# Performance work log

Measured on AMD Instinct MI355X. Metric: run time of the kernel, lower is better.

## Reference

```python
import jax, jax.numpy as jnp
import numpy as np

N = 100000      # nodes
E = 3200000     # edges (avg degree 32)
F_IN = 128      # data.num_features
H = 64          # hidden_channels
L = 64          # num_layers
C = 47          # data.num_classes
ALPHA = 0.1
THETA = 0.5


def setup_inputs() -> dict:
    key = jax.random.key(0)
    ks = jax.random.split(key, 8)
    x = jax.random.normal(ks[0], (N, F_IN), dtype=jnp.float32)
    edge_index = jax.random.randint(ks[1], (2, E), 0, N, dtype=jnp.int64)
    # Linear(F_IN, H), Linear(H, C), and L shared GCN2Conv weights [H, H]
    W1 = jax.random.normal(ks[2], (F_IN, H), dtype=jnp.float32) * 0.05
    b1 = jnp.zeros((H,), dtype=jnp.float32)
    conv_W = jax.random.normal(ks[3], (L, H, H), dtype=jnp.float32) * 0.05
    W2 = jax.random.normal(ks[4], (H, C), dtype=jnp.float32) * 0.05
    b2 = jnp.zeros((C,), dtype=jnp.float32)
    return {"x": x, "edge_index": edge_index, "W1": W1, "b1": b1,
            "conv_W": conv_W, "W2": W2, "b2": b2}


def reference(x, edge_index, W1, b1, conv_W, W2, b2):
    # --- normalized adjacency with renormalization trick: D^-1/2 (A + I) D^-1/2, transposed ---
    sl = jnp.arange(N, dtype=edge_index.dtype)
    r = jnp.concatenate([edge_index[1], sl])  # adj_t rows (destinations)
    c = jnp.concatenate([edge_index[0], sl])  # adj_t cols (sources)
    deg = jax.ops.segment_sum(jnp.ones((r.shape[0],), jnp.float32), r, num_segments=N)
    dinv = jax.lax.rsqrt(deg)                 # self-loops guarantee deg >= 1
    w = dinv[r] * dinv[c]                     # [E + N] edge weights

    def spmm(h):  # A_hat @ h via gather + segment scatter-add
        return jax.ops.segment_sum(w[:, None] * h[c], r, num_segments=N)

    # dropout is identity in eval mode
    x0 = jax.nn.relu(x @ W1 + b1)             # [N, H]
    betas = jnp.log(THETA / jnp.arange(1, L + 1, dtype=jnp.float32) + 1.0)

    def step(h, layer):
        Wl, beta = layer
        p = spmm(h)
        s = (1.0 - ALPHA) * p + ALPHA * x0    # initial-residual mix
        h = jax.nn.relu((1.0 - beta) * s + beta * (s @ Wl))  # identity mapping
        return h, None

    h, _ = jax.lax.scan(step, x0, (conv_W, betas))
    logits = h @ W2 + b2                      # [N, C]
    return jax.nn.log_softmax(logits, axis=-1)
```

## Files before the change

kernel.cpp:

```cpp
#include <hip/hip_runtime.h>
#include <hip/hip_bf16.h>
#include <hip/hip_fp16.h>
#include <math.h>

#define NN 100000
#define NE 3200000
#define FIN 128
#define HD 64
#define NL 64
#define NC 47
#define RPW 4
#define WPB 4
#define RPB (RPW * WPB)

#define NQ 4
#define NSEG 4
#define NKEY (NN * NQ)
#define KB ((NKEY + 1023) / 1024)

typedef float f32x4 __attribute__((ext_vector_type(4)));
typedef unsigned int u32x4 __attribute__((ext_vector_type(4)));


__device__ __forceinline__ float bf2f(unsigned short u) {
    union { unsigned int i; float f; } v; v.i = ((unsigned int)u) << 16; return v.f;
}
__device__ __forceinline__ unsigned short f2bf(float f) {
    __hip_bfloat16 h = __float2bfloat16(f);
    return *reinterpret_cast<unsigned short*>(&h);
}
__device__ __forceinline__ float bflo(unsigned int u) {
    union { unsigned int i; float f; } v; v.i = u << 16; return v.f;
}
__device__ __forceinline__ float bfhi(unsigned int u) {
    union { unsigned int i; float f; } v; v.i = u & 0xFFFF0000u; return v.f;
}
__device__ __forceinline__ unsigned int pack2h(float a, float b) {
    __half ha = __float2half(a), hb = __float2half(b);
    unsigned short ua = *reinterpret_cast<unsigned short*>(&ha);
    unsigned short ub = *reinterpret_cast<unsigned short*>(&hb);
    return (unsigned int)ua | ((unsigned int)ub << 16);
}
__device__ __forceinline__ float h2f(unsigned short u) {
    __half h = *reinterpret_cast<__half*>(&u);
    return __half2float(h);
}
__device__ __forceinline__ float fin_at(const void* p, int isf32, size_t i) {
    return isf32 ? ((const float*)p)[i]
                 : __bfloat162float(((const __hip_bfloat16*)p)[i]);
}
__device__ __forceinline__ int edge_at(const void* p, int is64, size_t i) {
    return is64 ? (int)((const long long*)p)[i] : ((const int*)p)[i];
}


__global__ void detect_kernel(const void* __restrict__ x, const void* __restrict__ eidx,
                              int* __restrict__ flags) {
    if (threadIdx.x == 0 && blockIdx.x == 0) {
        const unsigned short* u = (const unsigned short*)x;
        int sane = 0;
        for (int i = 0; i < 64; i++) {
            unsigned short v = u[2 * i];
            int e = (v >> 7) & 0xFF;
            if ((v & 0x7FFF) == 0 || (e >= 90 && e <= 141)) sane++;
        }
        flags[0] = (sane >= 48) ? 0 : 1;
        const int* e32 = (const int*)eidx;
        int nz = 0;
        for (int i = 0; i < 64; i++) if (e32[2 * i + 1] != 0) nz++;
        flags[1] = (nz == 0) ? 1 : 0;
    }
}


__global__ void key_count(const void* __restrict__ eidx, const int* __restrict__ flags,
                          int* __restrict__ cnt, int big) {
    int e = blockIdx.x * blockDim.x + threadIdx.x;
    if (e < NE) {
        int is64 = flags[1];
        int s = edge_at(eidx, is64, (size_t)e);
        int d = edge_at(eidx, is64, (size_t)NE + e);
        int q = s & 3;
        int key = big ? (q * NN + d) : (d * 4 + q);
        atomicAdd(&cnt[key], 1);
    }
}

__global__ __launch_bounds__(1024) void scan_reduce(const int* __restrict__ cnt,
                                                    int* __restrict__ bsum) {
    __shared__ int lds[1024];
    int tid = threadIdx.x;
    int i = blockIdx.x * 1024 + tid;
    lds[tid] = (i < NKEY) ? cnt[i] : 0;
    __syncthreads();
    for (int off = 512; off > 0; off >>= 1) {
        if (tid < off) lds[tid] += lds[tid + off];
        __syncthreads();
    }
    if (tid == 0) bsum[blockIdx.x] = lds[0];
}

__global__ __launch_bounds__(1024) void scan_mid(int* __restrict__ bsum, int* __restrict__ total_out) {
    __shared__ int lds[1024];
    __shared__ int base_s;
    int tid = threadIdx.x;
    if (tid == 0) base_s = 0;
    __syncthreads();
    for (int chunk = 0; chunk < KB; chunk += 1024) {
        int i = chunk + tid;
        int v = (i < KB) ? bsum[i] : 0;
        lds[tid] = v;
        __syncthreads();
        for (int off = 1; off < 1024; off <<= 1) {
            int t = (tid >= off) ? lds[tid - off] : 0;
            __syncthreads();
            lds[tid] += t;
            __syncthreads();
        }
        int incl = lds[tid];
        int base = base_s;
        if (i < KB) bsum[i] = base + incl - v;
        __syncthreads();
        if (tid == 1023) base_s = base + incl;
        __syncthreads();
    }
    if (tid == 0) *total_out = base_s;
}

__global__ __launch_bounds__(1024) void scan_final(const int* __restrict__ cnt,
                                                   const int* __restrict__ bsum,
                                                   int* __restrict__ keyptr) {
    __shared__ int lds[1024];
    int tid = threadIdx.x;
    int i = blockIdx.x * 1024 + tid;
    int v = (i < NKEY) ? cnt[i] : 0;
    lds[tid] = v;
    __syncthreads();
    for (int off = 1; off < 1024; off <<= 1) {
        int t = (tid >= off) ? lds[tid - off] : 0;
        __syncthreads();
        lds[tid] += t;
        __syncthreads();
    }
    if (i < NKEY) keyptr[i] = bsum[blockIdx.x] + lds[tid] - v;
}

__global__ void dinv_kernel(const int* __restrict__ keyptr, float* __restrict__ dinv, int big) {
    int i = blockIdx.x * blockDim.x + threadIdx.x;
    if (i < NN) {
        int deg;
        if (big) {
            deg = 0;
            #pragma unroll
            for (int q = 0; q < NQ; q++)
                deg += keyptr[q * NN + i + 1] - keyptr[q * NN + i];
        } else {
            deg = keyptr[(i + 1) * NSEG] - keyptr[i * NSEG];
        }
        dinv[i] = rsqrtf(1.0f + (float)deg);
    }
}

__global__ void scatter_kernel(const void* __restrict__ eidx, const int* __restrict__ flags,
                               const int* __restrict__ keyptr, int* __restrict__ fill,
                               int* __restrict__ col, int big) {
    int e = blockIdx.x * blockDim.x + threadIdx.x;
    if (e < NE) {
        int is64 = flags[1];
        int s = edge_at(eidx, is64, (size_t)e);
        int d = edge_at(eidx, is64, (size_t)NE + e);
        int q = s & 3;
        int key = big ? (q * NN + d) : (d * 4 + q);
        int pos = keyptr[key] + atomicAdd(&fill[key], 1);
        col[pos] = s;
    }
}


__global__ __launch_bounds__(256) void x0_kernel(const void* __restrict__ x,
                                                 const void* __restrict__ W1,
                                                 const void* __restrict__ b1,
                                                 const int* __restrict__ flags,
                                                 const float* __restrict__ dinv,
                                                 unsigned short* __restrict__ x0b,
                                                 unsigned short* __restrict__ g0) {
    __shared__ float lw[FIN * HD];
    int isf = flags[0];
    int tid = threadIdx.x;
    for (int i = tid; i < FIN * HD; i += 256) lw[i] = fin_at(W1, isf, i);
    __syncthreads();
    int wave = tid >> 6, lane = tid & 63;
    int row0 = blockIdx.x * RPB + wave * RPW;
    if (row0 >= NN) return;
    unsigned int pa01, pa23, pb01, pb23;
    {
        unsigned short a0 = f2bf(fin_at(x, isf, (size_t)(row0 + 0) * FIN + lane));
        unsigned short a1 = f2bf(fin_at(x, isf, (size_t)(row0 + 1) * FIN + lane));
        unsigned short a2 = f2bf(fin_at(x, isf, (size_t)(row0 + 2) * FIN + lane));
        unsigned short a3 = f2bf(fin_at(x, isf, (size_t)(row0 + 3) * FIN + lane));
        unsigned short c0 = f2bf(fin_at(x, isf, (size_t)(row0 + 0) * FIN + 64 + lane));
        unsigned short c1 = f2bf(fin_at(x, isf, (size_t)(row0 + 1) * FIN + 64 + lane));
        unsigned short c2 = f2bf(fin_at(x, isf, (size_t)(row0 + 2) * FIN + 64 + lane));
        unsigned short c3 = f2bf(fin_at(x, isf, (size_t)(row0 + 3) * FIN + 64 + lane));
        pa01 = ((unsigned int)a0 << 16) | a1;  pa23 = ((unsigned int)a2 << 16) | a3;
        pb01 = ((unsigned int)c0 << 16) | c1;  pb23 = ((unsigned int)c2 << 16) | c3;
    }
    float bias = fin_at(b1, isf, lane);
    float d0 = bias, d1 = bias, d2 = bias, d3 = bias;
    #pragma unroll 8
    for (int k = 0; k < 64; k++) {
        float w = lw[k * HD + lane];
        unsigned int b01 = __shfl(pa01, k, 64);
        unsigned int b23 = __shfl(pa23, k, 64);
        union { unsigned int i; float f; } f0, f1, f2, f3;
        f0.i = b01 & 0xFFFF0000u; f1.i = b01 << 16;
        f2.i = b23 & 0xFFFF0000u; f3.i = b23 << 16;
        d0 += f0.f * w; d1 += f1.f * w; d2 += f2.f * w; d3 += f3.f * w;
    }
    #pragma unroll 8
    for (int k = 0; k < 64; k++) {
        float w = lw[(64 + k) * HD + lane];
        unsigned int b01 = __shfl(pb01, k, 64);
        unsigned int b23 = __shfl(pb23, k, 64);
        union { unsigned int i; float f; } f0, f1, f2, f3;
        f0.i = b01 & 0xFFFF0000u; f1.i = b01 << 16;
        f2.i = b23 & 0xFFFF0000u; f3.i = b23 << 16;
        d0 += f0.f * w; d1 += f1.f * w; d2 += f2.f * w; d3 += f3.f * w;
    }
    float dd[RPW] = {d0, d1, d2, d3};
    #pragma unroll
    for (int r = 0; r < RPW; r++) {
        int row = row0 + r;
        if (row >= NN) continue;
        float v = fmaxf(dd[r], 0.0f);
        x0b[(size_t)row * HD + lane] = f2bf(v);
        g0[(size_t)row * HD + lane] = f2bf(dinv[row] * v);
    }
}


__global__ __launch_bounds__(256, 8) void spmm_partial(const int* __restrict__ keyptr,
                                                       const int* __restrict__ colq,
                                                       const unsigned short* __restrict__ g_in,
                                                       unsigned short* __restrict__ part) {
    int bid = blockIdx.x;
    int quad = bid & 3;
    int tile = bid >> 2;
    int tid = threadIdx.x;
    int wave = tid >> 6, lane = tid & 63;
    int grp = lane >> 3, li = lane & 7;
    int row = tile * 32 + wave * 8 + grp;
    size_t kbase = (size_t)quad * NN + row;
    int jbeg = keyptr[kbase];
    int jend = keyptr[kbase + 1];
    int cnt = jend - jbeg;
    const char* gb = (const char*)g_in;

    float a0 = 0.0f, a1 = 0.0f, a2 = 0.0f, a3 = 0.0f;
    float a4 = 0.0f, a5 = 0.0f, a6 = 0.0f, a7 = 0.0f;

    for (int base = 0; base < cnt; base += 8) {
        int idx = jbeg + base + li;
        int cv = colq[idx < jend ? idx : (jend - 1)];
        int rem = cnt - base;
        #pragma unroll
        for (int k = 0; k < 8; k++) {
            if (k < rem) {
                int ck = __shfl(cv, (lane & 56) + k, 64);
                uint4 u = *reinterpret_cast<const uint4*>(gb + (((size_t)ck) << 7) + (li << 4));
                a0 += bflo(u.x); a1 += bfhi(u.x);
                a2 += bflo(u.y); a3 += bfhi(u.y);
                a4 += bflo(u.z); a5 += bfhi(u.z);
                a6 += bflo(u.w); a7 += bfhi(u.w);
            }
        }
    }

    if (quad == (row & 3)) {
        uint4 u = *reinterpret_cast<const uint4*>(gb + (((size_t)row) << 7) + (li << 4));
        a0 += bflo(u.x); a1 += bfhi(u.x);
        a2 += bflo(u.y); a3 += bfhi(u.y);
        a4 += bflo(u.z); a5 += bfhi(u.z);
        a6 += bflo(u.w); a7 += bfhi(u.w);
    }

    u32x4 v = {pack2h(a0, a1), pack2h(a2, a3), pack2h(a4, a5), pack2h(a6, a7)};
    unsigned short* pp = part + kbase * HD + (li << 3);
    __builtin_nontemporal_store(v, reinterpret_cast<u32x4*>(pp));
}


__global__ __launch_bounds__(256, 8) void layer_combine(const unsigned short* __restrict__ part,
                                                        const float* __restrict__ dinv,
                                                        const unsigned short* __restrict__ x0b,
                                                        unsigned short* __restrict__ g_out,
                                                        const void* __restrict__ convW, int layer,
                                                        const int* __restrict__ flags, float beta) {
    __shared__ float lw[HD * HD];
    int isf = flags[0];
    size_t wbase = (size_t)layer * HD * HD;
    int tid = threadIdx.x;
    for (int i = tid; i < HD * HD; i += 256) lw[i] = fin_at(convW, isf, wbase + i);
    __syncthreads();

    int wave = __builtin_amdgcn_readfirstlane(tid >> 6);
    int lane = tid & 63;
    int row0 = blockIdx.x * RPB + wave * RPW;

    float sacc[RPW];
    float dsc[RPW];
    #pragma unroll
    for (int r = 0; r < RPW; r++) {
        int row = row0 + r;
        if (row >= NN) { sacc[r] = 0.0f; dsc[r] = 1.0f; continue; }
        float a = 0.0f;
        #pragma unroll
        for (int q = 0; q < NQ; q++) {
            unsigned short u = __builtin_nontemporal_load(
                part + ((size_t)q * NN + row) * HD + lane);
            a += h2f(u);
        }
        float di = dinv[row];
        dsc[r] = di;
        sacc[r] = 0.9f * (di * a) + 0.1f * bf2f(x0b[((size_t)row << 6) + lane]);
    }

    unsigned int p01 = ((unsigned int)f2bf(sacc[0]) << 16) | f2bf(sacc[1]);
    unsigned int p23 = ((unsigned int)f2bf(sacc[2]) << 16) | f2bf(sacc[3]);
    float d0 = 0.0f, d1 = 0.0f, d2 = 0.0f, d3 = 0.0f;
    #pragma unroll 8
    for (int k = 0; k < 64; k++) {
        float w = lw[k * HD + lane];
        unsigned int b01 = __shfl(p01, k, 64);
        unsigned int b23 = __shfl(p23, k, 64);
        union { unsigned int i; float f; } f0, f1, f2, f3;
        f0.i = b01 & 0xFFFF0000u; f1.i = b01 << 16;
        f2.i = b23 & 0xFFFF0000u; f3.i = b23 << 16;
        d0 += f0.f * w; d1 += f1.f * w;
        d2 += f2.f * w; d3 += f3.f * w;
    }

    float dd[RPW] = {d0, d1, d2, d3};
    float omb = 1.0f - beta;
    #pragma unroll
    for (int r = 0; r < RPW; r++) {
        int row = row0 + r;
        if (row >= NN) continue;
        float res = omb * sacc[r] + beta * dd[r];
        g_out[((size_t)row << 6) + lane] = f2bf(dsc[r] * fmaxf(res, 0.0f));
    }
}


__global__ __launch_bounds__(256, 8) void layer_fused(const int* __restrict__ keyptr,
                                                      const int* __restrict__ col,
                                                      const float* __restrict__ dinv,
                                                      const unsigned short* __restrict__ g_in,
                                                      const unsigned short* __restrict__ x0b,
                                                      unsigned short* __restrict__ g_out,
                                                      const void* __restrict__ convW, int layer,
                                                      const int* __restrict__ flags, float beta) {
    __shared__ float lw[HD * HD];
    int isf = flags[0];
    size_t wbase = (size_t)layer * HD * HD;
    int tid = threadIdx.x;
    for (int i = tid; i < HD * HD; i += 256) lw[i] = fin_at(convW, isf, wbase + i);
    __syncthreads();

    int wave = __builtin_amdgcn_readfirstlane(tid >> 6);
    int lane = tid & 63;
    int eslot = lane >> 3;
    int sbyte = (lane & 7) << 4;
    const char* gb = (const char*)g_in;

    int row0 = blockIdx.x * RPB + wave * RPW;

    float sacc[RPW];
    float dsc[RPW];
    #pragma unroll
    for (int r = 0; r < RPW; r++) {
        int row = row0 + r;
        if (row >= NN) { sacc[r] = 0.0f; dsc[r] = 1.0f; continue; }
        int start = keyptr[row * NSEG];
        int end   = keyptr[(row + 1) * NSEG];

        float a0 = 0.0f, a1 = 0.0f, a2 = 0.0f, a3 = 0.0f;
        float a4 = 0.0f, a5 = 0.0f, a6 = 0.0f, a7 = 0.0f;

        for (int j = start; j < end; j += 32) {
            int le = end - 1;
            int i0 = j + eslot, i1 = i0 + 8, i2 = i0 + 16, i3 = i0 + 24;
            int c0 = col[i0 < end ? i0 : le];
            int c1 = col[i1 < end ? i1 : le];
            int c2 = col[i2 < end ? i2 : le];
            int c3 = col[i3 < end ? i3 : le];
            uint4 u0 = *reinterpret_cast<const uint4*>(gb + (((size_t)c0) << 7) + sbyte);
            uint4 u1 = *reinterpret_cast<const uint4*>(gb + (((size_t)c1) << 7) + sbyte);
            uint4 u2 = *reinterpret_cast<const uint4*>(gb + (((size_t)c2) << 7) + sbyte);
            uint4 u3 = *reinterpret_cast<const uint4*>(gb + (((size_t)c3) << 7) + sbyte);
            float m0 = (i0 < end) ? 1.0f : 0.0f;
            float m1 = (i1 < end) ? 1.0f : 0.0f;
            float m2 = (i2 < end) ? 1.0f : 0.0f;
            float m3 = (i3 < end) ? 1.0f : 0.0f;
            a0 = fmaf(m0, bflo(u0.x), a0); a1 = fmaf(m0, bfhi(u0.x), a1);
            a2 = fmaf(m0, bflo(u0.y), a2); a3 = fmaf(m0, bfhi(u0.y), a3);
            a4 = fmaf(m0, bflo(u0.z), a4); a5 = fmaf(m0, bfhi(u0.z), a5);
            a6 = fmaf(m0, bflo(u0.w), a6); a7 = fmaf(m0, bfhi(u0.w), a7);
            a0 = fmaf(m1, bflo(u1.x), a0); a1 = fmaf(m1, bfhi(u1.x), a1);
            a2 = fmaf(m1, bflo(u1.y), a2); a3 = fmaf(m1, bfhi(u1.y), a3);
            a4 = fmaf(m1, bflo(u1.z), a4); a5 = fmaf(m1, bfhi(u1.z), a5);
            a6 = fmaf(m1, bflo(u1.w), a6); a7 = fmaf(m1, bfhi(u1.w), a7);
            a0 = fmaf(m2, bflo(u2.x), a0); a1 = fmaf(m2, bfhi(u2.x), a1);
            a2 = fmaf(m2, bflo(u2.y), a2); a3 = fmaf(m2, bfhi(u2.y), a3);
            a4 = fmaf(m2, bflo(u2.z), a4); a5 = fmaf(m2, bfhi(u2.z), a5);
            a6 = fmaf(m2, bflo(u2.w), a6); a7 = fmaf(m2, bfhi(u2.w), a7);
            a0 = fmaf(m3, bflo(u3.x), a0); a1 = fmaf(m3, bfhi(u3.x), a1);
            a2 = fmaf(m3, bflo(u3.y), a2); a3 = fmaf(m3, bfhi(u3.y), a3);
            a4 = fmaf(m3, bflo(u3.z), a4); a5 = fmaf(m3, bfhi(u3.z), a5);
            a6 = fmaf(m3, bflo(u3.w), a6); a7 = fmaf(m3, bfhi(u3.w), a7);
        }

        a0 += __shfl_xor(a0, 8, 64); a0 += __shfl_xor(a0, 16, 64); a0 += __shfl_xor(a0, 32, 64);
        a1 += __shfl_xor(a1, 8, 64); a1 += __shfl_xor(a1, 16, 64); a1 += __shfl_xor(a1, 32, 64);
        a2 += __shfl_xor(a2, 8, 64); a2 += __shfl_xor(a2, 16, 64); a2 += __shfl_xor(a2, 32, 64);
        a3 += __shfl_xor(a3, 8, 64); a3 += __shfl_xor(a3, 16, 64); a3 += __shfl_xor(a3, 32, 64);
        a4 += __shfl_xor(a4, 8, 64); a4 += __shfl_xor(a4, 16, 64); a4 += __shfl_xor(a4, 32, 64);
        a5 += __shfl_xor(a5, 8, 64); a5 += __shfl_xor(a5, 16, 64); a5 += __shfl_xor(a5, 32, 64);
        a6 += __shfl_xor(a6, 8, 64); a6 += __shfl_xor(a6, 16, 64); a6 += __shfl_xor(a6, 32, 64);
        a7 += __shfl_xor(a7, 8, 64); a7 += __shfl_xor(a7, 16, 64); a7 += __shfl_xor(a7, 32, 64);

        int srcl = lane >> 3;
        float t0 = __shfl(a0, srcl, 64);
        float t1 = __shfl(a1, srcl, 64);
        float t2 = __shfl(a2, srcl, 64);
        float t3 = __shfl(a3, srcl, 64);
        float t4 = __shfl(a4, srcl, 64);
        float t5 = __shfl(a5, srcl, 64);
        float t6 = __shfl(a6, srcl, 64);
        float t7 = __shfl(a7, srcl, 64);
        int b0 = lane & 1, b1 = (lane >> 1) & 1, b2 = (lane >> 2) & 1;
        float s01 = b0 ? t1 : t0, s23 = b0 ? t3 : t2;
        float s45 = b0 ? t5 : t4, s67 = b0 ? t7 : t6;
        float sA = b1 ? s23 : s01, sB = b1 ? s67 : s45;
        float gsum = b2 ? sB : sA;

        float a = gsum + bf2f(g_in[((size_t)row << 6) + lane]);
        float di = dinv[row];
        dsc[r] = di;
        sacc[r] = 0.9f * (di * a) + 0.1f * bf2f(x0b[((size_t)row << 6) + lane]);
    }

    unsigned int p01 = ((unsigned int)f2bf(sacc[0]) << 16) | f2bf(sacc[1]);
    unsigned int p23 = ((unsigned int)f2bf(sacc[2]) << 16) | f2bf(sacc[3]);
    float d0 = 0.0f, d1 = 0.0f, d2 = 0.0f, d3 = 0.0f;
    #pragma unroll 8
    for (int k = 0; k < 64; k++) {
        float w = lw[k * HD + lane];
        unsigned int b01 = __shfl(p01, k, 64);
        unsigned int b23 = __shfl(p23, k, 64);
        union { unsigned int i; float f; } f0, f1, f2, f3;
        f0.i = b01 & 0xFFFF0000u; f1.i = b01 << 16;
        f2.i = b23 & 0xFFFF0000u; f3.i = b23 << 16;
        d0 += f0.f * w; d1 += f1.f * w;
        d2 += f2.f * w; d3 += f3.f * w;
    }

    float dd[RPW] = {d0, d1, d2, d3};
    float omb = 1.0f - beta;
    #pragma unroll
    for (int r = 0; r < RPW; r++) {
        int row = row0 + r;
        if (row >= NN) continue;
        float res = omb * sacc[r] + beta * dd[r];
        g_out[((size_t)row << 6) + lane] = f2bf(dsc[r] * fmaxf(res, 0.0f));
    }
}


__global__ __launch_bounds__(256) void out_kernel(const unsigned short* __restrict__ g,
                                                  const float* __restrict__ dinv,
                                                  const void* __restrict__ W2,
                                                  const void* __restrict__ b2,
                                                  const int* __restrict__ flags,
                                                  void* __restrict__ out) {
    __shared__ float lw[HD * 64];
    int isf = flags[0];
    int tid = threadIdx.x;
    for (int i = tid; i < HD * 64; i += 256) {
        int k = i >> 6, j = i & 63;
        lw[i] = (j < NC) ? fin_at(W2, isf, (size_t)k * NC + j) : 0.0f;
    }
    __syncthreads();
    int row = blockIdx.x * 4 + (tid >> 6);
    int lane = tid & 63;
    if (row >= NN) return;
    float hv = bf2f(g[(size_t)row * HD + lane]) / dinv[row];
    float acc = (lane < NC) ? fin_at(b2, isf, lane) : 0.0f;
    #pragma unroll 8
    for (int k = 0; k < 64; k++) {
        float hk = __shfl(hv, k, 64);
        acc += hk * lw[k * 64 + lane];
    }
    float mv = (lane < NC) ? acc : -1e30f;
    for (int off = 32; off > 0; off >>= 1) mv = fmaxf(mv, __shfl_xor(mv, off, 64));
    float ex = (lane < NC) ? expf(acc - mv) : 0.0f;
    float se = ex;
    for (int off = 32; off > 0; off >>= 1) se += __shfl_xor(se, off, 64);
    float res = acc - mv - logf(se);
    if (lane < NC) {
        size_t oi = (size_t)row * NC + lane;
        if (isf) ((float*)out)[oi] = res;
        else     ((__hip_bfloat16*)out)[oi] = __float2bfloat16(res);
    }
}


static inline size_t align256(size_t x) { return (x + 255) & ~(size_t)255; }

extern "C" void kernel_launch(void* const* d_in, const int* in_sizes, int n_in,
                              void* d_out, int out_size, void* d_ws, size_t ws_size,
                              hipStream_t stream) {
    const void* x     = d_in[0];
    const void* eidx  = d_in[1];
    const void* W1    = d_in[2];
    const void* b1    = d_in[3];
    const void* convW = d_in[4];
    const void* W2    = d_in[5];
    const void* b2    = d_in[6];

    char* p = (char*)d_ws;
    size_t off = 0;
    auto alloc = [&](size_t bytes) { void* r = p + off; off += align256(bytes); return r; };
    int*            flags   = (int*)alloc(256);
    int*            cnt     = (int*)alloc((size_t)NKEY * 4);
    int*            fill    = (int*)alloc((size_t)NKEY * 4);
    int*            keyptr  = (int*)alloc((size_t)(NKEY + 1) * 4);
    int*            bsum    = (int*)alloc((size_t)KB * 4);
    float*          dinv    = (float*)alloc((size_t)NN * 4);
    int*            col     = (int*)alloc((size_t)NE * 4);
    unsigned short* x0b     = (unsigned short*)alloc((size_t)NN * HD * 2);
    unsigned short* hA      = (unsigned short*)alloc((size_t)NN * HD * 2);
    unsigned short* hB      = (unsigned short*)alloc((size_t)NN * HD * 2);

    size_t part_bytes = (size_t)NQ * NN * HD * 2;
    int big = (off + part_bytes) <= ws_size;
    unsigned short* part = (unsigned short*)(p + off);

    detect_kernel<<<1, 64, 0, stream>>>(x, eidx, flags);

    hipMemsetAsync(cnt, 0, (size_t)NKEY * 4, stream);
    hipMemsetAsync(fill, 0, (size_t)NKEY * 4, stream);
    key_count<<<(NE + 255) / 256, 256, 0, stream>>>(eidx, flags, cnt, big);
    scan_reduce<<<KB, 1024, 0, stream>>>(cnt, bsum);
    scan_mid<<<1, 1024, 0, stream>>>(bsum, keyptr + NKEY);
    scan_final<<<KB, 1024, 0, stream>>>(cnt, bsum, keyptr);
    dinv_kernel<<<(NN + 255) / 256, 256, 0, stream>>>(keyptr, dinv, big);
    scatter_kernel<<<(NE + 255) / 256, 256, 0, stream>>>(eidx, flags, keyptr, fill, col, big);

    int fb = (NN + RPB - 1) / RPB;
    x0_kernel<<<fb, 256, 0, stream>>>(x, W1, b1, flags, dinv, x0b, hA);

    unsigned short* gin = hA;
    unsigned short* gout = hB;
    for (int l = 0; l < NL; l++) {
        float beta = logf(0.5f / (float)(l + 1) + 1.0f);
        if (big) {
            spmm_partial<<<(NN / 32) * NQ, 256, 0, stream>>>(keyptr, col, gin, part);
            layer_combine<<<fb, 256, 0, stream>>>(part, dinv, x0b, gout,
                                                  convW, l, flags, beta);
        } else {
            layer_fused<<<fb, 256, 0, stream>>>(keyptr, col, dinv, gin, x0b, gout,
                                                convW, l, flags, beta);
        }
        unsigned short* t = gin; gin = gout; gout = t;
    }
    out_kernel<<<(NN + 3) / 4, 256, 0, stream>>>(gin, dinv, W2, b2, flags, (void*)d_out);
}
```

Measured before the change: 7.157 ms.

## Bind SpMM column quarters to XCDs via persistent work-stealing blocks

Turns spmm_partial into a persistent kernel with a fixed grid. Each block reads its XCC ID and pulls 32-row tiles from per-quarter atomic counters, starting with the quarter matching its XCD. The aim is that each XCD gathers mostly from one quarter of the feature table, so that quarter stays in that XCD's L2 and fewer gathers go to HBM or Infinity Cache. It adds atomic traffic, two block barriers per tile, and per-layer counters that must be zeroed.

```diff
diff --git a/kernel.cpp b/kernel.cpp
--- a/kernel.cpp
+++ b/kernel.cpp
@@ -17,6 +17,9 @@
 #define NSEG 4
 #define NKEY (NN * NQ)
 #define KB ((NKEY + 1023) / 1024)
+
+#define PGRID 2048
+#define NTILE 3125
 
 typedef float f32x4 __attribute__((ext_vector_type(4)));
 typedef unsigned int u32x4 __attribute__((ext_vector_type(4)));
@@ -242,51 +245,67 @@
 __global__ __launch_bounds__(256, 8) void spmm_partial(const int* __restrict__ keyptr,
                                                        const int* __restrict__ colq,
                                                        const unsigned short* __restrict__ g_in,
-                                                       unsigned short* __restrict__ part) {
-    int bid = blockIdx.x;
-    int quad = bid & 3;
-    int tile = bid >> 2;
+                                                       unsigned short* __restrict__ part,
+                                                       int* __restrict__ qcnt) {
+    unsigned int xcc;
+    asm volatile("s_getreg_b32 %0, hwreg(HW_REG_XCC_ID)" : "=s"(xcc));
+    int myq = (int)(xcc & 3);
+    __shared__ int tile_s;
     int tid = threadIdx.x;
     int wave = tid >> 6, lane = tid & 63;
     int grp = lane >> 3, li = lane & 7;
-    int row = tile * 32 + wave * 8 + grp;
-    size_t kbase = (size_t)quad * NN + row;
-    int jbeg = keyptr[kbase];
-    int jend = keyptr[kbase + 1];
-    int cnt = jend - jbeg;
     const char* gb = (const char*)g_in;
 
-    float a0 = 0.0f, a1 = 0.0f, a2 = 0.0f, a3 = 0.0f;
-    float a4 = 0.0f, a5 = 0.0f, a6 = 0.0f, a7 = 0.0f;
-
-    for (int base = 0; base < cnt; base += 8) {
-        int idx = jbeg + base + li;
-        int cv = colq[idx < jend ? idx : (jend - 1)];
-        int rem = cnt - base;
-        #pragma unroll
-        for (int k = 0; k < 8; k++) {
-            if (k < rem) {
-                int ck = __shfl(cv, (lane & 56) + k, 64);
-                uint4 u = *reinterpret_cast<const uint4*>(gb + (((size_t)ck) << 7) + (li << 4));
+    for (int qi = 0; qi < NQ; qi++) {
+        int quad = (myq + qi) & 3;
+        while (true) {
+            __syncthreads();
+            if (tid == 0) tile_s = atomicAdd(&qcnt[quad], 1);
+            __syncthreads();
+            int tile = tile_s;
+            if (tile >= NTILE) break;
+
+            int row = tile * 32 + wave * 8 + grp;
+            size_t kbase = (size_t)quad * NN + row;
+            int jbeg = keyptr[kbase];
+            int jend = keyptr[kbase + 1];
+            int cnt = jend - jbeg;
+
+            float a0 = 0.0f, a1 = 0.0f, a2 = 0.0f, a3 = 0.0f;
+            float a4 = 0.0f, a5 = 0.0f, a6 = 0.0f, a7 = 0.0f;
+
+            for (int base = 0; base < cnt; base += 8) {
+                int idx = jbeg + base + li;
+                int cv = colq[idx < jend ? idx : (jend - 1)];
+                int rem = cnt - base;
+                #pragma unroll
+                for (int k = 0; k < 8; k++) {
+                    if (k < rem) {
+                        int ck = __shfl(cv, (lane & 56) + k, 64);
+                        uint4 u = *reinterpret_cast<const uint4*>(
+                            gb + (((size_t)ck) << 7) + (li << 4));
+                        a0 += bflo(u.x); a1 += bfhi(u.x);
+                        a2 += bflo(u.y); a3 += bfhi(u.y);
+                        a4 += bflo(u.z); a5 += bfhi(u.z);
+                        a6 += bflo(u.w); a7 += bfhi(u.w);
+                    }
+                }
+            }
+
+            if (quad == (row & 3)) {
+                uint4 u = *reinterpret_cast<const uint4*>(
+                    gb + (((size_t)row) << 7) + (li << 4));
                 a0 += bflo(u.x); a1 += bfhi(u.x);
                 a2 += bflo(u.y); a3 += bfhi(u.y);
                 a4 += bflo(u.z); a5 += bfhi(u.z);
                 a6 += bflo(u.w); a7 += bfhi(u.w);
             }
-        }
-    }
-
-    if (quad == (row & 3)) {
-        uint4 u = *reinterpret_cast<const uint4*>(gb + (((size_t)row) << 7) + (li << 4));
-        a0 += bflo(u.x); a1 += bfhi(u.x);
-        a2 += bflo(u.y); a3 += bfhi(u.y);
-        a4 += bflo(u.z); a5 += bfhi(u.z);
-        a6 += bflo(u.w); a7 += bfhi(u.w);
-    }
-
-    u32x4 v = {pack2h(a0, a1), pack2h(a2, a3), pack2h(a4, a5), pack2h(a6, a7)};
-    unsigned short* pp = part + kbase * HD + (li << 3);
-    __builtin_nontemporal_store(v, reinterpret_cast<u32x4*>(pp));
+
+            u32x4 v = {pack2h(a0, a1), pack2h(a2, a3), pack2h(a4, a5), pack2h(a6, a7)};
+            unsigned short* pp = part + kbase * HD + (li << 3);
+            __builtin_nontemporal_store(v, reinterpret_cast<u32x4*>(pp));
+        }
+    }
 }
 
 
@@ -541,6 +560,7 @@
     unsigned short* x0b     = (unsigned short*)alloc((size_t)NN * HD * 2);
     unsigned short* hA      = (unsigned short*)alloc((size_t)NN * HD * 2);
     unsigned short* hB      = (unsigned short*)alloc((size_t)NN * HD * 2);
+    int*            qcnt    = (int*)alloc((size_t)NL * NQ * 4);
 
     size_t part_bytes = (size_t)NQ * NN * HD * 2;
     int big = (off + part_bytes) <= ws_size;
@@ -550,6 +570,7 @@
 
     hipMemsetAsync(cnt, 0, (size_t)NKEY * 4, stream);
     hipMemsetAsync(fill, 0, (size_t)NKEY * 4, stream);
+    hipMemsetAsync(qcnt, 0, (size_t)NL * NQ * 4, stream);
     key_count<<<(NE + 255) / 256, 256, 0, stream>>>(eidx, flags, cnt, big);
     scan_reduce<<<KB, 1024, 0, stream>>>(cnt, bsum);
     scan_mid<<<1, 1024, 0, stream>>>(bsum, keyptr + NKEY);
@@ -565,7 +586,7 @@
     for (int l = 0; l < NL; l++) {
         float beta = logf(0.5f / (float)(l + 1) + 1.0f);
         if (big) {
-            spmm_partial<<<(NN / 32) * NQ, 256, 0, stream>>>(keyptr, col, gin, part);
+            spmm_partial<<<PGRID, 256, 0, stream>>>(keyptr, col, gin, part, qcnt + l * NQ);
             layer_combine<<<fb, 256, 0, stream>>>(part, dinv, x0b, gout,
                                                   convW, l, flags, beta);
         } else {
```

Result: slower. 20.02 ms (+179.7%).
